# Optimization experiments

Hardware: AMD Instinct MI355X
Metric: run time of the kernel (lower is better)

The kernel has to match this reference:

```python
import jax, jax.numpy as jnp
import numpy as np

N, R, K = 4, 16384, 96


def setup_inputs() -> dict:
    key = jax.random.key(0)
    k1, k2, k3 = jax.random.split(key, 3)
    rgbs = jax.random.uniform(k1, (N, R, K, 3), dtype=jnp.float32)
    sigmas = jax.random.normal(k2, (N, R, K, 1), dtype=jnp.float32)
    # depths must be monotonically increasing along K (ray sample depths in [0.5, 3.5])
    depths = jnp.sort(0.5 + 3.0 * jax.random.uniform(k3, (N, R, K, 1), dtype=jnp.float32), axis=2)
    return {"rgbs": rgbs, "sigmas": sigmas, "depths": depths}


def reference(rgbs, sigmas, depths):
    # Default rendering_options: use_max_depth=False, no_dist=False,
    # use_mid_point=True, clamp_mode='mipnerf', last_back=False,
    # normalize_rgb=False, normalize_depth=True, clip_depth=True, white_back=False.
    deltas = depths[:, :, 1:] - depths[:, :, :-1]                  # [N,R,K-1,1]
    # midpoint averaging
    rgbs_m = 0.5 * (rgbs[:, :, :-1] + rgbs[:, :, 1:])              # [N,R,K-1,3]
    sigmas_m = 0.5 * (sigmas[:, :, :-1] + sigmas[:, :, 1:])        # [N,R,K-1,1]
    depths_m = 0.5 * (depths[:, :, :-1] + depths[:, :, 1:])        # [N,R,K-1,1]
    # mipnerf clamp: softplus(sigma - 1)
    sig = jax.nn.softplus(sigmas_m - 1.0)
    alphas = 1.0 - jnp.exp(-deltas * sig)                          # [N,R,K-1,1]
    # transmittance via exclusive cumprod along the sample axis
    alphas_shifted = jnp.concatenate(
        [jnp.ones_like(alphas[:, :, :1]), 1.0 - alphas + 1e-10], axis=-2)
    trans = jnp.cumprod(alphas_shifted, axis=-2)[:, :, :-1]        # [N,R,K-1,1]
    weights = alphas * trans                                       # [N,R,K-1,1]
    weights_sum = weights.sum(axis=2)                              # [N,R,1]
    composite_rgb = jnp.sum(weights * rgbs_m, axis=-2)             # [N,R,3]
    composite_depth = jnp.sum(weights * depths_m, axis=-2)         # [N,R,1]
    # normalize_depth=True
    composite_depth = composite_depth / weights_sum
    # clip_depth=True
    composite_depth = jnp.nan_to_num(composite_depth, nan=jnp.inf)
    composite_depth = jnp.clip(composite_depth, depths_m.min(), depths_m.max())
    composite_rgb = composite_rgb * 2.0 - 1.0
    return composite_rgb, composite_depth, weights
```

## Files before the change

### kernel.cpp

```cpp
#include <hip/hip_runtime.h>
#include <math.h>

#define NRAYS     65536
#define RGB_OFF   0
#define DEPTH_OFF (NRAYS * 3)
#define W_OFF     (NRAYS * 4)

#define RPB 16
#define SHD_OFF 0
#define SHS_OFF 1540
#define SHR_OFF 3080
#define SH_TOTAL 7696
#define WST_OFF 0
#define CST_OFF 1540
#define DST_OFF 1600

typedef float v4f __attribute__((ext_vector_type(4)));

#define DPPF(oldv, x, ctrl)                                                    \
    __int_as_float(__builtin_amdgcn_update_dpp(                                \
        __float_as_int(oldv), __float_as_int(x), (ctrl), 0xF, 0xF, false))

__device__ __forceinline__ float one_minus_alpha(float x, float delta) {
    const float L2E = 1.44269504088896340736f;
    float xl = x * L2E;
    float l2 = (x > 20.0f) ? xl
                           : __builtin_amdgcn_logf(1.0f + __builtin_amdgcn_exp2f(xl));
    return __builtin_amdgcn_exp2f(-delta * l2);
}

__device__ __forceinline__ void gload_lds16(const float* g, float* l) {
    __builtin_amdgcn_global_load_lds(
        (const __attribute__((address_space(1))) void*)g,
        (__attribute__((address_space(3))) void*)l, 16, 0, 2);
}

__global__ __launch_bounds__(256) void integrate_kernel(
    const float* __restrict__ rgbs,
    const float* __restrict__ sigmas,
    const float* __restrict__ depths,
    float* __restrict__ out)
{
    __shared__ float sh[SH_TOTAL];

    const int t   = threadIdx.x;
    const int w   = t >> 6;
    const int l64 = t & 63;
    const int blk = ((blockIdx.x & 7) << 9) | (blockIdx.x >> 3);

    {
        const float* gd = depths + (size_t)blk * (RPB * 96);
        const float* gs = sigmas + (size_t)blk * (RPB * 96);
        const float* gr = rgbs   + (size_t)blk * (RPB * 288);
        for (int c = w; c < 30; c += 4) {
            const float* src; float* dst;
            if (c < 6)       { src = gd + c * 256;        dst = sh + SHD_OFF + c * 256; }
            else if (c < 12) { src = gs + (c - 6) * 256;  dst = sh + SHS_OFF + (c - 6) * 256; }
            else             { src = gr + (c - 12) * 256; dst = sh + SHR_OFF + (c - 12) * 256; }
            gload_lds16(src + l64 * 4, dst + l64 * 4);
        }
    }
    __builtin_amdgcn_s_waitcnt(0x0F70);
    __syncthreads();

    const int rb_ = t >> 4;
    const int l   = t & 15;
    const bool full = (l < 15);

    const float* db = sh + SHD_OFF + rb_ * 96  + 6 * l;
    const float* sp = sh + SHS_OFF + rb_ * 96  + 6 * l;
    const float* rp = sh + SHR_OFF + rb_ * 288 + 18 * l;

    float2 e0 = *(const float2*)(db);
    float2 e1 = *(const float2*)(db + 2);
    float2 e2 = *(const float2*)(db + 4);
    float2 e3 = *(const float2*)(db + 6);
    float2 f0 = *(const float2*)(sp);
    float2 f1 = *(const float2*)(sp + 2);
    float2 f2v = *(const float2*)(sp + 4);
    float2 f3 = *(const float2*)(sp + 6);
    float2 c0 = *(const float2*)(rp);
    float2 c1 = *(const float2*)(rp + 2);
    float2 c2 = *(const float2*)(rp + 4);
    float2 c3 = *(const float2*)(rp + 6);
    float2 c4 = *(const float2*)(rp + 8);
    float2 c5 = *(const float2*)(rp + 10);
    float2 c6 = *(const float2*)(rp + 12);
    float2 c7 = *(const float2*)(rp + 14);
    float2 c8 = *(const float2*)(rp + 16);
    float2 c9 = *(const float2*)(rp + 18);
    float  r20 = rp[20];

    __syncthreads();

    const float D[7] = {e0.x, e0.y, e1.x, e1.y, e2.x, e2.y, e3.x};
    const float S[7] = {f0.x, f0.y, f1.x, f1.y, f2v.x, f2v.y, f3.x};
    const float R[7] = {c0.x, c1.y, c3.x, c4.y, c6.x, c7.y, c9.x};
    const float G[7] = {c0.y, c2.x, c3.y, c5.x, c6.y, c8.x, c9.y};
    const float B[7] = {c1.x, c2.y, c4.x, c5.y, c7.x, c8.y, r20};

    float u[6];
    float Tloc = 1.0f;
    float Sw = 0.f, Sd = 0.f, Sr = 0.f, Sg = 0.f, Sbv = 0.f;

#define DO_IV(I)                                                      \
    { float delta = D[(I)+1] - D[I];                                  \
      float x = 0.5f * (S[I] + S[(I)+1]) - 1.0f;                      \
      float e = one_minus_alpha(x, delta);                            \
      float uu = (1.0f - e) * Tloc;                                   \
      Tloc *= e + 1e-10f;                                             \
      u[I] = uu;                                                      \
      Sw  += uu;                                                      \
      Sd  += uu * (0.5f * (D[I] + D[(I)+1]));                         \
      Sr  += uu * (0.5f * (R[I] + R[(I)+1]));                         \
      Sg  += uu * (0.5f * (G[I] + G[(I)+1]));                         \
      Sbv += uu * (0.5f * (B[I] + B[(I)+1])); }

    DO_IV(0) DO_IV(1) DO_IV(2) DO_IV(3) DO_IV(4)
    if (full) { DO_IV(5) } else { u[5] = 0.f; }
#undef DO_IV

    float incl = Tloc;
    incl *= DPPF(1.0f, incl, 0x111);
    incl *= DPPF(1.0f, incl, 0x112);
    incl *= DPPF(1.0f, incl, 0x114);
    incl *= DPPF(1.0f, incl, 0x118);
    float Tin = DPPF(1.0f, incl, 0x111);

    Sw *= Tin; Sd *= Tin; Sr *= Tin; Sg *= Tin; Sbv *= Tin;

#define RED(v)                         \
    v += DPPF(0.f, v, 0x111);          \
    v += DPPF(0.f, v, 0x112);          \
    v += DPPF(0.f, v, 0x114);          \
    v += DPPF(0.f, v, 0x118);
    RED(Sw) RED(Sd) RED(Sr) RED(Sg) RED(Sbv)
#undef RED

    float lo0 = 0.5f * (D[0] + D[1]);
    float lo  = DPPF(0.f, lo0, 0x11F);

    {
        float* wst = sh + WST_OFF + rb_ * 95 + 6 * l;
        float2* wst2 = (float2*)wst;
        wst2[0] = float2{Tin * u[0], Tin * u[1]};
        wst2[1] = float2{Tin * u[2], Tin * u[3]};
        if (full) wst2[2] = float2{Tin * u[4], Tin * u[5]};
        else      wst[4]  = Tin * u[4];
    }
    if (l == 15) {
        sh[CST_OFF + rb_ * 3 + 0] = 2.f * Sr  - 1.f;
        sh[CST_OFF + rb_ * 3 + 1] = 2.f * Sg  - 1.f;
        sh[CST_OFF + rb_ * 3 + 2] = 2.f * Sbv - 1.f;
        float dv = Sd / Sw;
        float hi = 0.5f * (D[4] + D[5]);
        dv = fmaxf(fminf(dv, hi), lo);
        sh[DST_OFF + rb_] = dv;
    }
    __syncthreads();

    {
        v4f* dst = (v4f*)(out + W_OFF + (size_t)blk * (RPB * 95));
        const v4f* src = (const v4f*)(sh + WST_OFF);
        __builtin_nontemporal_store(src[t], dst + t);
        if (t < 124) __builtin_nontemporal_store(src[256 + t], dst + 256 + t);
    }
    if (t < 12) {
        __builtin_nontemporal_store(
            ((const v4f*)(sh + CST_OFF))[t],
            (v4f*)(out + RGB_OFF + (size_t)blk * (RPB * 3)) + t);
    }
    if (t < 4) {
        __builtin_nontemporal_store(
            ((const v4f*)(sh + DST_OFF))[t],
            (v4f*)(out + DEPTH_OFF + (size_t)blk * RPB) + t);
    }
}

extern "C" void kernel_launch(void* const* d_in, const int* in_sizes, int n_in,
                              void* d_out, int out_size, void* d_ws, size_t ws_size,
                              hipStream_t stream) {
    const float* rgbs   = (const float*)d_in[0];
    const float* sigmas = (const float*)d_in[1];
    const float* depths = (const float*)d_in[2];
    float* out = (float*)d_out;

    integrate_kernel<<<NRAYS / RPB, 256, 0, stream>>>(rgbs, sigmas, depths, out);
}
```

Measured before the change: 149.9 us.

## Make blocks persistent over eight tiles with double-buffered async LDS staging

Each block now processes eight consecutive ray tiles instead of one. The global-to-LDS load of the next tile is issued before computing the current one into a second LDS buffer, with hand-counted vmcnt waits per wave. This aims to overlap memory latency with compute and cut block launch overhead. In exchange it doubles LDS per block, which lowers occupancy, and it relies on fragile manual waitcnt values that also count outstanding stores, which risks correctness or stalls.

New measurement: 153.8 us. +2.6%, slower.

```diff
diff --git a/kernel.cpp b/kernel.cpp
--- a/kernel.cpp
+++ b/kernel.cpp
@@ -15,11 +15,19 @@
 #define CST_OFF 1540
 #define DST_OFF 1600
 
+#define TPB 8
+#define NBLOCKS (NRAYS / RPB / TPB)
+
 typedef float v4f __attribute__((ext_vector_type(4)));
 
 #define DPPF(oldv, x, ctrl)                                                    \
     __int_as_float(__builtin_amdgcn_update_dpp(                                \
         __float_as_int(oldv), __float_as_int(x), (ctrl), 0xF, 0xF, false))
+
+#define WAITVM(N) asm volatile("s_waitcnt vmcnt(" #N ")" ::: "memory")
+#define LGKM0     asm volatile("s_waitcnt lgkmcnt(0)" ::: "memory")
+#define BARRIER()                                                              \
+    do { __builtin_amdgcn_s_barrier(); asm volatile("" ::: "memory"); } while (0)
 
 __device__ __forceinline__ float one_minus_alpha(float x, float delta) {
     const float L2E = 1.44269504088896340736f;
@@ -35,145 +43,173 @@
         (__attribute__((address_space(3))) void*)l, 16, 0, 2);
 }
 
+__device__ __forceinline__ void stage_tile(const float* __restrict__ rgbs,
+                                           const float* __restrict__ sigmas,
+                                           const float* __restrict__ depths,
+                                           int tile, float* buf, int w, int l64) {
+    const float* gd = depths + (size_t)tile * (RPB * 96);
+    const float* gs = sigmas + (size_t)tile * (RPB * 96);
+    const float* gr = rgbs   + (size_t)tile * (RPB * 288);
+    for (int c = w; c < 30; c += 4) {
+        const float* src; float* dst;
+        if (c < 6)       { src = gd + c * 256;        dst = buf + SHD_OFF + c * 256; }
+        else if (c < 12) { src = gs + (c - 6) * 256;  dst = buf + SHS_OFF + (c - 6) * 256; }
+        else             { src = gr + (c - 12) * 256; dst = buf + SHR_OFF + (c - 12) * 256; }
+        gload_lds16(src + l64 * 4, dst + l64 * 4);
+    }
+}
+
 __global__ __launch_bounds__(256) void integrate_kernel(
     const float* __restrict__ rgbs,
     const float* __restrict__ sigmas,
     const float* __restrict__ depths,
     float* __restrict__ out)
 {
-    __shared__ float sh[SH_TOTAL];
+    __shared__ float sh[2 * SH_TOTAL];
 
     const int t   = threadIdx.x;
     const int w   = t >> 6;
     const int l64 = t & 63;
-    const int blk = ((blockIdx.x & 7) << 9) | (blockIdx.x >> 3);
-
-    {
-        const float* gd = depths + (size_t)blk * (RPB * 96);
-        const float* gs = sigmas + (size_t)blk * (RPB * 96);
-        const float* gr = rgbs   + (size_t)blk * (RPB * 288);
-        for (int c = w; c < 30; c += 4) {
-            const float* src; float* dst;
-            if (c < 6)       { src = gd + c * 256;        dst = sh + SHD_OFF + c * 256; }
-            else if (c < 12) { src = gs + (c - 6) * 256;  dst = sh + SHS_OFF + (c - 6) * 256; }
-            else             { src = gr + (c - 12) * 256; dst = sh + SHR_OFF + (c - 12) * 256; }
-            gload_lds16(src + l64 * 4, dst + l64 * 4);
-        }
-    }
-    __builtin_amdgcn_s_waitcnt(0x0F70);
-    __syncthreads();
+    const int tile0 = ((blockIdx.x & 7) << 9) | ((blockIdx.x >> 3) << 3);
 
     const int rb_ = t >> 4;
     const int l   = t & 15;
     const bool full = (l < 15);
 
-    const float* db = sh + SHD_OFF + rb_ * 96  + 6 * l;
-    const float* sp = sh + SHS_OFF + rb_ * 96  + 6 * l;
-    const float* rp = sh + SHR_OFF + rb_ * 288 + 18 * l;
-
-    float2 e0 = *(const float2*)(db);
-    float2 e1 = *(const float2*)(db + 2);
-    float2 e2 = *(const float2*)(db + 4);
-    float2 e3 = *(const float2*)(db + 6);
-    float2 f0 = *(const float2*)(sp);
-    float2 f1 = *(const float2*)(sp + 2);
-    float2 f2v = *(const float2*)(sp + 4);
-    float2 f3 = *(const float2*)(sp + 6);
-    float2 c0 = *(const float2*)(rp);
-    float2 c1 = *(const float2*)(rp + 2);
-    float2 c2 = *(const float2*)(rp + 4);
-    float2 c3 = *(const float2*)(rp + 6);
-    float2 c4 = *(const float2*)(rp + 8);
-    float2 c5 = *(const float2*)(rp + 10);
-    float2 c6 = *(const float2*)(rp + 12);
-    float2 c7 = *(const float2*)(rp + 14);
-    float2 c8 = *(const float2*)(rp + 16);
-    float2 c9 = *(const float2*)(rp + 18);
-    float  r20 = rp[20];
-
-    __syncthreads();
-
-    const float D[7] = {e0.x, e0.y, e1.x, e1.y, e2.x, e2.y, e3.x};
-    const float S[7] = {f0.x, f0.y, f1.x, f1.y, f2v.x, f2v.y, f3.x};
-    const float R[7] = {c0.x, c1.y, c3.x, c4.y, c6.x, c7.y, c9.x};
-    const float G[7] = {c0.y, c2.x, c3.y, c5.x, c6.y, c8.x, c9.y};
-    const float B[7] = {c1.x, c2.y, c4.x, c5.y, c7.x, c8.y, r20};
-
-    float u[6];
-    float Tloc = 1.0f;
-    float Sw = 0.f, Sd = 0.f, Sr = 0.f, Sg = 0.f, Sbv = 0.f;
+    stage_tile(rgbs, sigmas, depths, tile0, sh, w, l64);
+
+    for (int i = 0; i < TPB; ++i) {
+        float* buf = sh + (i & 1) * SH_TOTAL;
+        const int tile = tile0 + i;
+
+        if (i < TPB - 1)
+            stage_tile(rgbs, sigmas, depths, tile + 1, sh + ((i + 1) & 1) * SH_TOTAL, w, l64);
+
+        if (i == 0) {
+            if (w < 2) { WAITVM(8); } else { WAITVM(7); }
+        } else if (i < TPB - 1) {
+            if      (w == 0) { WAITVM(12); }
+            else if (w == 1) { WAITVM(10); }
+            else             { WAITVM(8);  }
+        } else {
+            if      (w == 0) { WAITVM(4); }
+            else if (w == 1) { WAITVM(2); }
+            else             { WAITVM(1); }
+        }
+        BARRIER();
+
+        const float* db = buf + SHD_OFF + rb_ * 96  + 6 * l;
+        const float* sp = buf + SHS_OFF + rb_ * 96  + 6 * l;
+        const float* rp = buf + SHR_OFF + rb_ * 288 + 18 * l;
+
+        float2 e0 = *(const float2*)(db);
+        float2 e1 = *(const float2*)(db + 2);
+        float2 e2 = *(const float2*)(db + 4);
+        float2 e3 = *(const float2*)(db + 6);
+        float2 f0 = *(const float2*)(sp);
+        float2 f1 = *(const float2*)(sp + 2);
+        float2 f2v = *(const float2*)(sp + 4);
+        float2 f3 = *(const float2*)(sp + 6);
+        float2 c0 = *(const float2*)(rp);
+        float2 c1 = *(const float2*)(rp + 2);
+        float2 c2 = *(const float2*)(rp + 4);
+        float2 c3 = *(const float2*)(rp + 6);
+        float2 c4 = *(const float2*)(rp + 8);
+        float2 c5 = *(const float2*)(rp + 10);
+        float2 c6 = *(const float2*)(rp + 12);
+        float2 c7 = *(const float2*)(rp + 14);
+        float2 c8 = *(const float2*)(rp + 16);
+        float2 c9 = *(const float2*)(rp + 18);
+        float  r20 = rp[20];
+
+        LGKM0;
+        BARRIER();
+
+        const float D[7] = {e0.x, e0.y, e1.x, e1.y, e2.x, e2.y, e3.x};
+        const float S[7] = {f0.x, f0.y, f1.x, f1.y, f2v.x, f2v.y, f3.x};
+        const float R[7] = {c0.x, c1.y, c3.x, c4.y, c6.x, c7.y, c9.x};
+        const float G[7] = {c0.y, c2.x, c3.y, c5.x, c6.y, c8.x, c9.y};
+        const float B[7] = {c1.x, c2.y, c4.x, c5.y, c7.x, c8.y, r20};
+
+        float u[6];
+        float Tloc = 1.0f;
+        float Sw = 0.f, Sd = 0.f, Sr = 0.f, Sg = 0.f, Sbv = 0.f;
 
 #define DO_IV(I)                                                      \
-    { float delta = D[(I)+1] - D[I];                                  \
-      float x = 0.5f * (S[I] + S[(I)+1]) - 1.0f;                      \
-      float e = one_minus_alpha(x, delta);                            \
-      float uu = (1.0f - e) * Tloc;                                   \
-      Tloc *= e + 1e-10f;                                             \
-      u[I] = uu;                                                      \
-      Sw  += uu;                                                      \
-      Sd  += uu * (0.5f * (D[I] + D[(I)+1]));                         \
-      Sr  += uu * (0.5f * (R[I] + R[(I)+1]));                         \
-      Sg  += uu * (0.5f * (G[I] + G[(I)+1]));                         \
-      Sbv += uu * (0.5f * (B[I] + B[(I)+1])); }
-
-    DO_IV(0) DO_IV(1) DO_IV(2) DO_IV(3) DO_IV(4)
-    if (full) { DO_IV(5) } else { u[5] = 0.f; }
+        { float delta = D[(I)+1] - D[I];                              \
+          float x = 0.5f * (S[I] + S[(I)+1]) - 1.0f;                  \
+          float e = one_minus_alpha(x, delta);                        \
+          float uu = (1.0f - e) * Tloc;                               \
+          Tloc *= e + 1e-10f;                                         \
+          u[I] = uu;                                                  \
+          Sw  += uu;                                                  \
+          Sd  += uu * (0.5f * (D[I] + D[(I)+1]));                     \
+          Sr  += uu * (0.5f * (R[I] + R[(I)+1]));                     \
+          Sg  += uu * (0.5f * (G[I] + G[(I)+1]));                     \
+          Sbv += uu * (0.5f * (B[I] + B[(I)+1])); }
+
+        DO_IV(0) DO_IV(1) DO_IV(2) DO_IV(3) DO_IV(4)
+        if (full) { DO_IV(5) } else { u[5] = 0.f; }
 #undef DO_IV
 
-    float incl = Tloc;
-    incl *= DPPF(1.0f, incl, 0x111);
-    incl *= DPPF(1.0f, incl, 0x112);
-    incl *= DPPF(1.0f, incl, 0x114);
-    incl *= DPPF(1.0f, incl, 0x118);
-    float Tin = DPPF(1.0f, incl, 0x111);
-
-    Sw *= Tin; Sd *= Tin; Sr *= Tin; Sg *= Tin; Sbv *= Tin;
+        float incl = Tloc;
+        incl *= DPPF(1.0f, incl, 0x111);
+        incl *= DPPF(1.0f, incl, 0x112);
+        incl *= DPPF(1.0f, incl, 0x114);
+        incl *= DPPF(1.0f, incl, 0x118);
+        float Tin = DPPF(1.0f, incl, 0x111);
+
+        Sw *= Tin; Sd *= Tin; Sr *= Tin; Sg *= Tin; Sbv *= Tin;
 
 #define RED(v)                         \
-    v += DPPF(0.f, v, 0x111);          \
-    v += DPPF(0.f, v, 0x112);          \
-    v += DPPF(0.f, v, 0x114);          \
-    v += DPPF(0.f, v, 0x118);
-    RED(Sw) RED(Sd) RED(Sr) RED(Sg) RED(Sbv)
+        v += DPPF(0.f, v, 0x111);      \
+        v += DPPF(0.f, v, 0x112);      \
+        v += DPPF(0.f, v, 0x114);      \
+        v += DPPF(0.f, v, 0x118);
+        RED(Sw) RED(Sd) RED(Sr) RED(Sg) RED(Sbv)
 #undef RED
 
-    float lo0 = 0.5f * (D[0] + D[1]);
-    float lo  = DPPF(0.f, lo0, 0x11F);
-
-    {
-        float* wst = sh + WST_OFF + rb_ * 95 + 6 * l;
-        float2* wst2 = (float2*)wst;
-        wst2[0] = float2{Tin * u[0], Tin * u[1]};
-        wst2[1] = float2{Tin * u[2], Tin * u[3]};
-        if (full) wst2[2] = float2{Tin * u[4], Tin * u[5]};
-        else      wst[4]  = Tin * u[4];
-    }
-    if (l == 15) {
-        sh[CST_OFF + rb_ * 3 + 0] = 2.f * Sr  - 1.f;
-        sh[CST_OFF + rb_ * 3 + 1] = 2.f * Sg  - 1.f;
-        sh[CST_OFF + rb_ * 3 + 2] = 2.f * Sbv - 1.f;
-        float dv = Sd / Sw;
-        float hi = 0.5f * (D[4] + D[5]);
-        dv = fmaxf(fminf(dv, hi), lo);
-        sh[DST_OFF + rb_] = dv;
-    }
-    __syncthreads();
-
-    {
-        v4f* dst = (v4f*)(out + W_OFF + (size_t)blk * (RPB * 95));
-        const v4f* src = (const v4f*)(sh + WST_OFF);
-        __builtin_nontemporal_store(src[t], dst + t);
-        if (t < 124) __builtin_nontemporal_store(src[256 + t], dst + 256 + t);
-    }
-    if (t < 12) {
-        __builtin_nontemporal_store(
-            ((const v4f*)(sh + CST_OFF))[t],
-            (v4f*)(out + RGB_OFF + (size_t)blk * (RPB * 3)) + t);
-    }
-    if (t < 4) {
-        __builtin_nontemporal_store(
-            ((const v4f*)(sh + DST_OFF))[t],
-            (v4f*)(out + DEPTH_OFF + (size_t)blk * RPB) + t);
+        float lo0 = 0.5f * (D[0] + D[1]);
+        float lo  = DPPF(0.f, lo0, 0x11F);
+
+        {
+            float* wst = buf + WST_OFF + rb_ * 95 + 6 * l;
+            float2* wst2 = (float2*)wst;
+            wst2[0] = float2{Tin * u[0], Tin * u[1]};
+            wst2[1] = float2{Tin * u[2], Tin * u[3]};
+            if (full) wst2[2] = float2{Tin * u[4], Tin * u[5]};
+            else      wst[4]  = Tin * u[4];
+        }
+        if (l == 15) {
+            buf[CST_OFF + rb_ * 3 + 0] = 2.f * Sr  - 1.f;
+            buf[CST_OFF + rb_ * 3 + 1] = 2.f * Sg  - 1.f;
+            buf[CST_OFF + rb_ * 3 + 2] = 2.f * Sbv - 1.f;
+            float dv = Sd / Sw;
+            float hi = 0.5f * (D[4] + D[5]);
+            dv = fmaxf(fminf(dv, hi), lo);
+            buf[DST_OFF + rb_] = dv;
+        }
+        LGKM0;
+        BARRIER();
+
+        {
+            v4f* dst = (v4f*)(out + W_OFF + (size_t)tile * (RPB * 95));
+            const v4f* src = (const v4f*)(buf + WST_OFF);
+            __builtin_nontemporal_store(src[t], dst + t);
+            if (t < 124) __builtin_nontemporal_store(src[256 + t], dst + 256 + t);
+        }
+        if (t < 12) {
+            __builtin_nontemporal_store(
+                ((const v4f*)(buf + CST_OFF))[t],
+                (v4f*)(out + RGB_OFF + (size_t)tile * (RPB * 3)) + t);
+        }
+        if (t < 4) {
+            __builtin_nontemporal_store(
+                ((const v4f*)(buf + DST_OFF))[t],
+                (v4f*)(out + DEPTH_OFF + (size_t)tile * RPB) + t);
+        }
+        LGKM0;
+        BARRIER();
     }
 }
 
@@ -185,5 +221,5 @@
     const float* depths = (const float*)d_in[2];
     float* out = (float*)d_out;
 
-    integrate_kernel<<<NRAYS / RPB, 256, 0, stream>>>(rgbs, sigmas, depths, out);
-}
+    integrate_kernel<<<NBLOCKS, 256, 0, stream>>>(rgbs, sigmas, depths, out);
+}
```

## Make each wave load and store its own rays and drop block-wide barriers

Applied to the files above, without the earlier changes.

Each wavefront now loads only the depth, sigma and rgb data of its own four rays into LDS, splits the loads into two ordered groups, and waits on vmcnt so the transmittance math runs while the rgb loads are still in flight. All __syncthreads are replaced by per-wave waitcnt, and the weight and composite staging reuses the wave's own LDS region, so each wave writes its outputs on its own. This removes block-level synchronisation and overlaps compute with memory. The cost is more, smaller 4-byte LDS-DMA loads and reliance on hand-placed waitcnt and sched_barrier ordering for correctness.

After: 148.8 us, median of 2. About the same (-0.8%).

```diff
diff --git a/kernel.cpp b/kernel.cpp
--- a/kernel.cpp
+++ b/kernel.cpp
@@ -11,15 +11,18 @@
 #define SHS_OFF 1540
 #define SHR_OFF 3080
 #define SH_TOTAL 7696
-#define WST_OFF 0
-#define CST_OFF 1540
-#define DST_OFF 1600
 
 typedef float v4f __attribute__((ext_vector_type(4)));
 
 #define DPPF(oldv, x, ctrl)                                                    \
     __int_as_float(__builtin_amdgcn_update_dpp(                                \
         __float_as_int(oldv), __float_as_int(x), (ctrl), 0xF, 0xF, false))
+
+#define WAITVM(N) asm volatile("s_waitcnt vmcnt(" #N ")" ::: "memory")
+#define LGKM0     asm volatile("s_waitcnt lgkmcnt(0)" ::: "memory")
+#define SCHED_PIN()                                                            \
+    do { asm volatile("" ::: "memory");                                        \
+         __builtin_amdgcn_sched_barrier(0); } while (0)
 
 __device__ __forceinline__ float one_minus_alpha(float x, float delta) {
     const float L2E = 1.44269504088896340736f;
@@ -33,6 +36,11 @@
     __builtin_amdgcn_global_load_lds(
         (const __attribute__((address_space(1))) void*)g,
         (__attribute__((address_space(3))) void*)l, 16, 0, 2);
+}
+__device__ __forceinline__ void gload_lds4(const float* g, float* l) {
+    __builtin_amdgcn_global_load_lds(
+        (const __attribute__((address_space(1))) void*)g,
+        (__attribute__((address_space(3))) void*)l, 4, 0, 2);
 }
 
 __global__ __launch_bounds__(256) void integrate_kernel(
@@ -49,27 +57,40 @@
     const int blk = ((blockIdx.x & 7) << 9) | (blockIdx.x >> 3);
 
     {
-        const float* gd = depths + (size_t)blk * (RPB * 96);
-        const float* gs = sigmas + (size_t)blk * (RPB * 96);
-        const float* gr = rgbs   + (size_t)blk * (RPB * 288);
-        for (int c = w; c < 30; c += 4) {
-            const float* src; float* dst;
-            if (c < 6)       { src = gd + c * 256;        dst = sh + SHD_OFF + c * 256; }
-            else if (c < 12) { src = gs + (c - 6) * 256;  dst = sh + SHS_OFF + (c - 6) * 256; }
-            else             { src = gr + (c - 12) * 256; dst = sh + SHR_OFF + (c - 12) * 256; }
-            gload_lds16(src + l64 * 4, dst + l64 * 4);
-        }
-    }
-    __builtin_amdgcn_s_waitcnt(0x0F70);
-    __syncthreads();
-
-    const int rb_ = t >> 4;
-    const int l   = t & 15;
+        const float* gd = depths + (size_t)blk * (RPB * 96)  + w * 384;
+        const float* gs = sigmas + (size_t)blk * (RPB * 96)  + w * 384;
+        const float* gr = rgbs   + (size_t)blk * (RPB * 288) + w * 1152;
+        float* dd  = sh + SHD_OFF + w * 384;
+        float* dsg = sh + SHS_OFF + w * 384;
+        float* dr  = sh + SHR_OFF + w * 1152;
+
+        gload_lds16(gd + l64 * 4, dd + l64 * 4);
+        gload_lds4 (gd + 256 + l64, dd + 256 + l64);
+        gload_lds4 (gd + 320 + l64, dd + 320 + l64);
+        gload_lds16(gs + l64 * 4, dsg + l64 * 4);
+        gload_lds4 (gs + 256 + l64, dsg + 256 + l64);
+        gload_lds4 (gs + 320 + l64, dsg + 320 + l64);
+
+        SCHED_PIN();
+
+#pragma unroll
+        for (int c = 0; c < 4; ++c)
+            gload_lds16(gr + c * 256 + l64 * 4, dr + c * 256 + l64 * 4);
+        gload_lds4(gr + 1024 + l64, dr + 1024 + l64);
+        gload_lds4(gr + 1088 + l64, dr + 1088 + l64);
+
+        SCHED_PIN();
+    }
+
+    const int rb_  = t >> 4;
+    const int rloc = rb_ & 3;
+    const int l    = t & 15;
     const bool full = (l < 15);
 
-    const float* db = sh + SHD_OFF + rb_ * 96  + 6 * l;
-    const float* sp = sh + SHS_OFF + rb_ * 96  + 6 * l;
-    const float* rp = sh + SHR_OFF + rb_ * 288 + 18 * l;
+    WAITVM(6);
+
+    const float* db = sh + SHD_OFF + rb_ * 96 + 6 * l;
+    const float* sp = sh + SHS_OFF + rb_ * 96 + 6 * l;
 
     float2 e0 = *(const float2*)(db);
     float2 e1 = *(const float2*)(db + 2);
@@ -79,6 +100,50 @@
     float2 f1 = *(const float2*)(sp + 2);
     float2 f2v = *(const float2*)(sp + 4);
     float2 f3 = *(const float2*)(sp + 6);
+    LGKM0;
+
+    const float D[7] = {e0.x, e0.y, e1.x, e1.y, e2.x, e2.y, e3.x};
+    const float S[7] = {f0.x, f0.y, f1.x, f1.y, f2v.x, f2v.y, f3.x};
+
+    float u[6];
+    float Tloc = 1.0f;
+    float Sw = 0.f, Sd = 0.f;
+
+#define DO_A(I)                                                       \
+    { float delta = D[(I)+1] - D[I];                                  \
+      float x = 0.5f * (S[I] + S[(I)+1]) - 1.0f;                      \
+      float e = one_minus_alpha(x, delta);                            \
+      float uu = (1.0f - e) * Tloc;                                   \
+      Tloc *= e + 1e-10f;                                             \
+      u[I] = uu;                                                      \
+      Sw  += uu;                                                      \
+      Sd  += uu * (0.5f * (D[I] + D[(I)+1])); }
+
+    DO_A(0) DO_A(1) DO_A(2) DO_A(3) DO_A(4)
+    if (full) { DO_A(5) } else { u[5] = 0.f; }
+#undef DO_A
+
+    float incl = Tloc;
+    incl *= DPPF(1.0f, incl, 0x111);
+    incl *= DPPF(1.0f, incl, 0x112);
+    incl *= DPPF(1.0f, incl, 0x114);
+    incl *= DPPF(1.0f, incl, 0x118);
+    float Tin = DPPF(1.0f, incl, 0x111);
+
+    Sw *= Tin; Sd *= Tin;
+
+#define RED(v)                         \
+    v += DPPF(0.f, v, 0x111);          \
+    v += DPPF(0.f, v, 0x112);          \
+    v += DPPF(0.f, v, 0x114);          \
+    v += DPPF(0.f, v, 0x118);
+    RED(Sw) RED(Sd)
+
+    float lo0 = 0.5f * (D[0] + D[1]);
+    float lo  = DPPF(0.f, lo0, 0x11F);
+
+    WAITVM(0);
+    const float* rp = sh + SHR_OFF + rb_ * 288 + 18 * l;
     float2 c0 = *(const float2*)(rp);
     float2 c1 = *(const float2*)(rp + 2);
     float2 c2 = *(const float2*)(rp + 4);
@@ -90,58 +155,27 @@
     float2 c8 = *(const float2*)(rp + 16);
     float2 c9 = *(const float2*)(rp + 18);
     float  r20 = rp[20];
-
-    __syncthreads();
-
-    const float D[7] = {e0.x, e0.y, e1.x, e1.y, e2.x, e2.y, e3.x};
-    const float S[7] = {f0.x, f0.y, f1.x, f1.y, f2v.x, f2v.y, f3.x};
+    LGKM0;
+
     const float R[7] = {c0.x, c1.y, c3.x, c4.y, c6.x, c7.y, c9.x};
     const float G[7] = {c0.y, c2.x, c3.y, c5.x, c6.y, c8.x, c9.y};
     const float B[7] = {c1.x, c2.y, c4.x, c5.y, c7.x, c8.y, r20};
 
-    float u[6];
-    float Tloc = 1.0f;
-    float Sw = 0.f, Sd = 0.f, Sr = 0.f, Sg = 0.f, Sbv = 0.f;
-
-#define DO_IV(I)                                                      \
-    { float delta = D[(I)+1] - D[I];                                  \
-      float x = 0.5f * (S[I] + S[(I)+1]) - 1.0f;                      \
-      float e = one_minus_alpha(x, delta);                            \
-      float uu = (1.0f - e) * Tloc;                                   \
-      Tloc *= e + 1e-10f;                                             \
-      u[I] = uu;                                                      \
-      Sw  += uu;                                                      \
-      Sd  += uu * (0.5f * (D[I] + D[(I)+1]));                         \
-      Sr  += uu * (0.5f * (R[I] + R[(I)+1]));                         \
-      Sg  += uu * (0.5f * (G[I] + G[(I)+1]));                         \
-      Sbv += uu * (0.5f * (B[I] + B[(I)+1])); }
-
-    DO_IV(0) DO_IV(1) DO_IV(2) DO_IV(3) DO_IV(4)
-    if (full) { DO_IV(5) } else { u[5] = 0.f; }
-#undef DO_IV
-
-    float incl = Tloc;
-    incl *= DPPF(1.0f, incl, 0x111);
-    incl *= DPPF(1.0f, incl, 0x112);
-    incl *= DPPF(1.0f, incl, 0x114);
-    incl *= DPPF(1.0f, incl, 0x118);
-    float Tin = DPPF(1.0f, incl, 0x111);
-
-    Sw *= Tin; Sd *= Tin; Sr *= Tin; Sg *= Tin; Sbv *= Tin;
-
-#define RED(v)                         \
-    v += DPPF(0.f, v, 0x111);          \
-    v += DPPF(0.f, v, 0x112);          \
-    v += DPPF(0.f, v, 0x114);          \
-    v += DPPF(0.f, v, 0x118);
-    RED(Sw) RED(Sd) RED(Sr) RED(Sg) RED(Sbv)
+    float Sr = 0.f, Sg = 0.f, Sbv = 0.f;
+#define DO_B(I)                                                       \
+    { Sr  += u[I] * (0.5f * (R[I] + R[(I)+1]));                       \
+      Sg  += u[I] * (0.5f * (G[I] + G[(I)+1]));                       \
+      Sbv += u[I] * (0.5f * (B[I] + B[(I)+1])); }
+    DO_B(0) DO_B(1) DO_B(2) DO_B(3) DO_B(4)
+    if (full) { DO_B(5) }
+#undef DO_B
+
+    Sr *= Tin; Sg *= Tin; Sbv *= Tin;
+    RED(Sr) RED(Sg) RED(Sbv)
 #undef RED
 
-    float lo0 = 0.5f * (D[0] + D[1]);
-    float lo  = DPPF(0.f, lo0, 0x11F);
-
     {
-        float* wst = sh + WST_OFF + rb_ * 95 + 6 * l;
+        float* wst = sh + SHD_OFF + w * 384 + rloc * 95 + 6 * l;
         float2* wst2 = (float2*)wst;
         wst2[0] = float2{Tin * u[0], Tin * u[1]};
         wst2[1] = float2{Tin * u[2], Tin * u[3]};
@@ -149,31 +183,32 @@
         else      wst[4]  = Tin * u[4];
     }
     if (l == 15) {
-        sh[CST_OFF + rb_ * 3 + 0] = 2.f * Sr  - 1.f;
-        sh[CST_OFF + rb_ * 3 + 1] = 2.f * Sg  - 1.f;
-        sh[CST_OFF + rb_ * 3 + 2] = 2.f * Sbv - 1.f;
+        float* cst = sh + SHS_OFF + w * 384;
+        cst[rloc * 3 + 0] = 2.f * Sr  - 1.f;
+        cst[rloc * 3 + 1] = 2.f * Sg  - 1.f;
+        cst[rloc * 3 + 2] = 2.f * Sbv - 1.f;
         float dv = Sd / Sw;
         float hi = 0.5f * (D[4] + D[5]);
         dv = fmaxf(fminf(dv, hi), lo);
-        sh[DST_OFF + rb_] = dv;
-    }
-    __syncthreads();
+        cst[12 + rloc] = dv;
+    }
+    LGKM0;
 
     {
-        v4f* dst = (v4f*)(out + W_OFF + (size_t)blk * (RPB * 95));
-        const v4f* src = (const v4f*)(sh + WST_OFF);
-        __builtin_nontemporal_store(src[t], dst + t);
-        if (t < 124) __builtin_nontemporal_store(src[256 + t], dst + 256 + t);
-    }
-    if (t < 12) {
+        const v4f* src = (const v4f*)(sh + SHD_OFF + w * 384);
+        v4f* dst = (v4f*)(out + W_OFF + ((size_t)blk * RPB + 4 * w) * 95);
+        __builtin_nontemporal_store(src[l64], dst + l64);
+        if (l64 < 31) __builtin_nontemporal_store(src[64 + l64], dst + 64 + l64);
+    }
+    if (l64 < 3) {
         __builtin_nontemporal_store(
-            ((const v4f*)(sh + CST_OFF))[t],
-            (v4f*)(out + RGB_OFF + (size_t)blk * (RPB * 3)) + t);
-    }
-    if (t < 4) {
+            ((const v4f*)(sh + SHS_OFF + w * 384))[l64],
+            (v4f*)(out + RGB_OFF + ((size_t)blk * RPB + 4 * w) * 3) + l64);
+    }
+    if (l64 == 3) {
         __builtin_nontemporal_store(
-            ((const v4f*)(sh + DST_OFF))[t],
-            (v4f*)(out + DEPTH_OFF + (size_t)blk * RPB) + t);
+            ((const v4f*)(sh + SHS_OFF + w * 384 + 12))[0],
+            (v4f*)(out + DEPTH_OFF + (size_t)blk * RPB + 4 * w));
     }
 }
 
```
